# Performance work log

Measured on AMD Instinct MI355X. Metric: run time of the kernel, lower is better.

## Reference

```python
import jax, jax.numpy as jnp
import numpy as np

B, IN, OUT = 256, 1024, 1024


def choquet_cardinal(z):
    """Discrete Choquet integral over last axis with cardinality measure mu(A)=|A|/n.
    ChI(x) = sum_i (x_(i) - x_(i-1)) * mu(A_i), x_(0)=0, mu(A_i)=(n-i+1)/n.
    """
    n = z.shape[-1]
    xs = jnp.sort(z, axis=-1)  # ascending
    # diffs[..., 0] = x_(1); diffs[..., i] = x_(i+1) - x_(i)
    diffs = jnp.concatenate([xs[..., :1], jnp.diff(xs, axis=-1)], axis=-1)
    mu = (n - jnp.arange(n, dtype=xs.dtype)) / n  # 1, (n-1)/n, ..., 1/n
    return jnp.einsum('...i,i->...', diffs, mu)


def setup_inputs() -> dict:
    key = jax.random.key(0)
    kx, kw, kb = jax.random.split(key, 3)
    x = jax.random.normal(kx, (B, 1, IN), dtype=jnp.float32)
    weight = jax.random.normal(kw, (IN, OUT), dtype=jnp.float32) * 0.02
    bias = jax.random.normal(kb, (IN, OUT), dtype=jnp.float32) * 0.02
    return {"x": x, "weight": weight, "bias": bias}


def reference(x, weight, bias):
    # z: [B, OUT, IN] = x * W^T + b^T (elementwise with broadcast)
    z = x * weight.T + bias.T
    chi = choquet_cardinal(z)  # [B, OUT]
    return jax.nn.sigmoid(chi)
```

## Files before the change

kernel.cpp:

```cpp
#include <hip/hip_runtime.h>
#include <math.h>


#define BATCH   256
#define IN_DIM  1024
#define OUT_DIM 1024

typedef __bf16 bf16x8 __attribute__((ext_vector_type(8)));
typedef float  f32x4  __attribute__((ext_vector_type(4)));

__global__ __launch_bounds__(256) void chad_fused(
    const float* __restrict__ x,
    const float* __restrict__ w,
    const float* __restrict__ bias,
    float* __restrict__ out)
{
    __shared__ float red[4][64][4];
    __shared__ float bsum[16][16];

    const int t    = threadIdx.x;
    const int lane = t & 63;
    const int wv   = t >> 6;
    const int l16  = lane & 15;
    const int quad = lane >> 4;
    const int mt   = blockIdx.x >> 6;
    const int nt   = blockIdx.x & 63;

    const float* ap = x + (size_t)(mt * 16 + l16) * IN_DIM + wv * 256 + quad * 8;
    const float* bp = w + (size_t)(wv * 256 + quad * 8) * OUT_DIM + nt * 16 + l16;

    f32x4 acc = {0.f, 0.f, 0.f, 0.f};
    #pragma unroll
    for (int i = 0; i < 8; ++i) {
        const float4 a0 = *(const float4*)(ap + i * 32);
        const float4 a1 = *(const float4*)(ap + i * 32 + 4);
        const float* bpi = bp + (size_t)i * 32 * OUT_DIM;
        float bv[8];
        #pragma unroll
        for (int j = 0; j < 8; ++j) bv[j] = bpi[(size_t)j * OUT_DIM];
        bf16x8 af, bfv;
        af[0] = (__bf16)a0.x; af[1] = (__bf16)a0.y;
        af[2] = (__bf16)a0.z; af[3] = (__bf16)a0.w;
        af[4] = (__bf16)a1.x; af[5] = (__bf16)a1.y;
        af[6] = (__bf16)a1.z; af[7] = (__bf16)a1.w;
        #pragma unroll
        for (int j = 0; j < 8; ++j) bfv[j] = (__bf16)bv[j];
        acc = __builtin_amdgcn_mfma_f32_16x16x32_bf16(af, bfv, acc, 0, 0, 0);
    }
    *(f32x4*)&red[wv][lane][0] = acc;

    {
        const int rg = t >> 4;
        const float* bb = bias + (size_t)rg * 64 * OUT_DIM + nt * 16 + (t & 15);
        float s = 0.f;
        #pragma unroll 8
        for (int r = 0; r < 64; ++r) s += bb[(size_t)r * OUT_DIM];
        bsum[rg][t & 15] = s;
    }
    __syncthreads();

    const int row = t >> 4, col = t & 15;
    const int rl  = ((row >> 2) << 4) + col;
    const int rr  = row & 3;
    float v = red[0][rl][rr] + red[1][rl][rr] + red[2][rl][rr] + red[3][rl][rr];
    float cs = 0.f;
    #pragma unroll
    for (int p = 0; p < 16; ++p) cs += bsum[p][col];
    v = (v + cs) * (1.0f / (float)IN_DIM);
    out[(size_t)(mt * 16 + row) * OUT_DIM + nt * 16 + col] = 1.0f / (1.0f + __expf(-v));
}

extern "C" void kernel_launch(void* const* d_in, const int* in_sizes, int n_in,
                              void* d_out, int out_size, void* d_ws, size_t ws_size,
                              hipStream_t stream) {
    const float* x  = (const float*)d_in[0];
    const float* w  = (const float*)d_in[1];
    const float* b  = (const float*)d_in[2];
    chad_fused<<<(BATCH / 16) * (OUT_DIM / 16), 256, 0, stream>>>(
        x, w, b, (float*)d_out);
}
```

Measured before the change: 77.58 us.

## Stage 32x32 tiles of x and W in LDS as bf16 before MFMA

Each block now covers a 32x32 output tile instead of 16x16 and preloads the full K range of x and W into shared memory as bf16, with padded rows. Wave-level MFMAs then read their operands from LDS. W and bias are fetched with coalesced float4 row loads rather than strided scalar column loads, and the bias column sums are folded into the same loop. The aim is to cut redundant global traffic and uncoalesced accesses. The cost is roughly 130KB of LDS per block, which limits occupancy to about one block per CU, and the grid shrinks to 256 blocks.

```diff
diff --git a/kernel.cpp b/kernel.cpp
--- a/kernel.cpp
+++ b/kernel.cpp
@@ -6,6 +6,11 @@
 #define IN_DIM  1024
 #define OUT_DIM 1024
 
+#define BM 32
+#define BN 32
+#define KP (IN_DIM + 8)
+
+typedef __bf16 bf16x4 __attribute__((ext_vector_type(4)));
 typedef __bf16 bf16x8 __attribute__((ext_vector_type(8)));
 typedef float  f32x4  __attribute__((ext_vector_type(4)));
 
@@ -15,59 +20,86 @@
     const float* __restrict__ bias,
     float* __restrict__ out)
 {
-    __shared__ float red[4][64][4];
-    __shared__ float bsum[16][16];
+    __shared__ __bf16 Alds[BM][KP];
+    __shared__ __bf16 Blds[BN][KP];
+    __shared__ float  bscr[32][32];
+    __shared__ float  csum[BN];
 
     const int t    = threadIdx.x;
     const int lane = t & 63;
     const int wv   = t >> 6;
     const int l16  = lane & 15;
     const int quad = lane >> 4;
-    const int mt   = blockIdx.x >> 6;
-    const int nt   = blockIdx.x & 63;
-
-    const float* ap = x + (size_t)(mt * 16 + l16) * IN_DIM + wv * 256 + quad * 8;
-    const float* bp = w + (size_t)(wv * 256 + quad * 8) * OUT_DIM + nt * 16 + l16;
-
-    f32x4 acc = {0.f, 0.f, 0.f, 0.f};
-    #pragma unroll
-    for (int i = 0; i < 8; ++i) {
-        const float4 a0 = *(const float4*)(ap + i * 32);
-        const float4 a1 = *(const float4*)(ap + i * 32 + 4);
-        const float* bpi = bp + (size_t)i * 32 * OUT_DIM;
-        float bv[8];
-        #pragma unroll
-        for (int j = 0; j < 8; ++j) bv[j] = bpi[(size_t)j * OUT_DIM];
-        bf16x8 af, bfv;
-        af[0] = (__bf16)a0.x; af[1] = (__bf16)a0.y;
-        af[2] = (__bf16)a0.z; af[3] = (__bf16)a0.w;
-        af[4] = (__bf16)a1.x; af[5] = (__bf16)a1.y;
-        af[6] = (__bf16)a1.z; af[7] = (__bf16)a1.w;
-        #pragma unroll
-        for (int j = 0; j < 8; ++j) bfv[j] = (__bf16)bv[j];
-        acc = __builtin_amdgcn_mfma_f32_16x16x32_bf16(af, bfv, acc, 0, 0, 0);
-    }
-    *(f32x4*)&red[wv][lane][0] = acc;
+    const int mt   = blockIdx.x >> 5;
+    const int nt   = blockIdx.x & 31;
 
     {
-        const int rg = t >> 4;
-        const float* bb = bias + (size_t)rg * 64 * OUT_DIM + nt * 16 + (t & 15);
-        float s = 0.f;
-        #pragma unroll 8
-        for (int r = 0; r < 64; ++r) s += bb[(size_t)r * OUT_DIM];
-        bsum[rg][t & 15] = s;
+        const float* xs = x + (size_t)(mt * BM) * IN_DIM + t * 4;
+        #pragma unroll 4
+        for (int it = 0; it < 32; ++it) {
+            const float4 v = *(const float4*)(xs + (size_t)it * IN_DIM);
+            bf16x4 o = { (__bf16)v.x, (__bf16)v.y, (__bf16)v.z, (__bf16)v.w };
+            *(bf16x4*)&Alds[it][t * 4] = o;
+        }
+    }
+
+    {
+        const int kb = 2 * (t >> 3);
+        const int c  = 4 * (t & 7);
+        const float* wsrc = w    + (size_t)kb * OUT_DIM + nt * BN + c;
+        const float* bsrc = bias + (size_t)kb * OUT_DIM + nt * BN + c;
+        f32x4 bacc = {0.f, 0.f, 0.f, 0.f};
+        #pragma unroll 4
+        for (int it = 0; it < 16; ++it) {
+            const size_t roff = (size_t)it * 64 * OUT_DIM;
+            const float4 w0 = *(const float4*)(wsrc + roff);
+            const float4 w1 = *(const float4*)(wsrc + roff + OUT_DIM);
+            const float4 b0 = *(const float4*)(bsrc + roff);
+            const float4 b1 = *(const float4*)(bsrc + roff + OUT_DIM);
+            const int k = it * 64 + kb;
+            #pragma unroll
+            for (int i = 0; i < 4; ++i) {
+                union { __bf16 h[2]; unsigned int u; } p;
+                p.h[0] = (__bf16)((&w0.x)[i]);
+                p.h[1] = (__bf16)((&w1.x)[i]);
+                *(unsigned int*)&Blds[c + i][k] = p.u;
+            }
+            bacc[0] += b0.x + b1.x;
+            bacc[1] += b0.y + b1.y;
+            bacc[2] += b0.z + b1.z;
+            bacc[3] += b0.w + b1.w;
+        }
+        *(f32x4*)&bscr[t >> 3][c] = bacc;
     }
     __syncthreads();
 
-    const int row = t >> 4, col = t & 15;
-    const int rl  = ((row >> 2) << 4) + col;
-    const int rr  = row & 3;
-    float v = red[0][rl][rr] + red[1][rl][rr] + red[2][rl][rr] + red[3][rl][rr];
-    float cs = 0.f;
+    if (t < BN) {
+        float s = 0.f;
+        #pragma unroll
+        for (int g = 0; g < 32; ++g) s += bscr[g][t];
+        csum[t] = s;
+    }
+
+    const __bf16* ab = &Alds[(wv >> 1) * 16 + l16][quad * 8];
+    const __bf16* bb = &Blds[(wv &  1) * 16 + l16][quad * 8];
+    f32x4 acc = {0.f, 0.f, 0.f, 0.f};
     #pragma unroll
-    for (int p = 0; p < 16; ++p) cs += bsum[p][col];
-    v = (v + cs) * (1.0f / (float)IN_DIM);
-    out[(size_t)(mt * 16 + row) * OUT_DIM + nt * 16 + col] = 1.0f / (1.0f + __expf(-v));
+    for (int s = 0; s < 32; ++s) {
+        const bf16x8 af = *(const bf16x8*)(ab + s * 32);
+        const bf16x8 bf = *(const bf16x8*)(bb + s * 32);
+        acc = __builtin_amdgcn_mfma_f32_16x16x32_bf16(af, bf, acc, 0, 0, 0);
+    }
+    __syncthreads();
+
+    const float cs   = csum[(wv & 1) * 16 + l16];
+    const int  orow0 = mt * BM + (wv >> 1) * 16 + quad * 4;
+    const int  ocol  = nt * BN + (wv &  1) * 16 + l16;
+    float* op = out + (size_t)orow0 * OUT_DIM + ocol;
+    #pragma unroll
+    for (int r = 0; r < 4; ++r) {
+        const float v = (acc[r] + cs) * (1.0f / (float)IN_DIM);
+        op[(size_t)r * OUT_DIM] = 1.0f / (1.0f + __expf(-v));
+    }
 }
 
 extern "C" void kernel_launch(void* const* d_in, const int* in_sizes, int n_in,
@@ -76,6 +108,6 @@
     const float* x  = (const float*)d_in[0];
     const float* w  = (const float*)d_in[1];
     const float* b  = (const float*)d_in[2];
-    chad_fused<<<(BATCH / 16) * (OUT_DIM / 16), 256, 0, stream>>>(
+    chad_fused<<<(BATCH / BM) * (OUT_DIM / BN), 256, 0, stream>>>(
         x, w, b, (float*)d_out);
 }
```

Result: faster. 69.21 us (-10.8%).
